# Optimization experiments

Hardware: AMD Instinct MI355X
Metric: run time of the kernel (lower is better)

## Reference

```python
import jax, jax.numpy as jnp
import numpy as np

B, T, D = 64, 512, 384
MAX_LEN = 4096


def setup_inputs() -> dict:
    key = jax.random.key(0)
    kx, kd = jax.random.split(key)
    x = jax.random.normal(kx, (B, T, D), dtype=jnp.float32)
    duration = jax.random.randint(kd, (B, T), 0, 8, dtype=jnp.int32)
    return {"x": x, "duration": duration, "max_len": MAX_LEN}


def reference(x, duration, max_len):
    # x: [B, T, D], duration: [B, T] int, max_len: python int
    # Cumsum trick replaces the per-row repeat_interleave + cat + pad:
    # token t of row b occupies output rows [csum[t-1], csum[t]).
    csum = jnp.cumsum(duration, axis=1)                       # [B, T]
    mel_len = csum[:, -1]                                     # [B]
    pos = jnp.arange(max_len, dtype=csum.dtype)               # [M]
    # For each output position m, index of source token: first t with csum[t] > m
    idx = jax.vmap(lambda c: jnp.searchsorted(c, pos, side="right"))(csum)  # [B, M]
    idx = jnp.minimum(idx, x.shape[1] - 1)
    out = jnp.take_along_axis(x, idx[:, :, None], axis=1)     # [B, M, D]
    mask = (pos[None, :] < mel_len[:, None])[:, :, None]      # [B, M, 1]
    out = jnp.where(mask, out, jnp.zeros((), dtype=out.dtype))
    return out, mel_len
```

## Files before the change

### kernel.cpp

```cpp
#include <hip/hip_runtime.h>


#define T_DIM 512
#define D_DIM 384
#define D4    (D_DIM / 4)
#define ROWS  32
#define BLOCK 512

__global__ __launch_bounds__(BLOCK) void length_regulator_kernel(
    const float* __restrict__ x,
    const int*   __restrict__ duration,
    float*       __restrict__ out,
    int B, int ML)
{
    __shared__ int s_csum[T_DIM];
    __shared__ int s_idx[ROWS];

    const int chunks_per_b = ML / ROWS;
    const int b     = blockIdx.x / chunks_per_b;
    const int chunk = blockIdx.x % chunks_per_b;
    const int row0  = chunk * ROWS;
    const int tid   = threadIdx.x;

    s_csum[tid] = duration[b * T_DIM + tid];
    __syncthreads();

    for (int off = 1; off < T_DIM; off <<= 1) {
        int v = (tid >= off) ? s_csum[tid - off] : 0;
        __syncthreads();
        s_csum[tid] += v;
        __syncthreads();
    }
    const int mel = s_csum[T_DIM - 1];

    if (tid < ROWS) {
        const int pos = row0 + tid;
        int idx;
        if (pos >= mel) {
            idx = -1;
        } else {
            int lo = 0, hi = T_DIM;
            while (lo < hi) {
                int mid = (lo + hi) >> 1;
                if (s_csum[mid] <= pos) lo = mid + 1; else hi = mid;
            }
            idx = (lo < T_DIM - 1) ? lo : (T_DIM - 1);
        }
        s_idx[tid] = idx;
    }
    __syncthreads();

    const float4* __restrict__ x4   = (const float4*)x;
    float4*       __restrict__ out4 = (float4*)out;
    const float4 zero = make_float4(0.f, 0.f, 0.f, 0.f);

    const long long out_base = ((long long)b * ML + row0) * D4;
    const long long x_base   = (long long)b * T_DIM * D4;

    #pragma unroll
    for (int i = 0; i < (ROWS * D4) / BLOCK; ++i) {
        const int flat = tid + i * BLOCK;
        const int r = flat / D4;
        const int j = flat - r * D4;
        const int t = s_idx[r];
        float4 v = (t < 0) ? zero : x4[x_base + (long long)t * D4 + j];
        out4[out_base + flat] = v;
    }

    if (chunk == 0 && tid == 0) {
        out[(long long)B * ML * D_DIM + b] = (float)mel;
    }
}

extern "C" void kernel_launch(void* const* d_in, const int* in_sizes, int n_in,
                              void* d_out, int out_size, void* d_ws, size_t ws_size,
                              hipStream_t stream) {
    const float* x   = (const float*)d_in[0];
    const int*   dur = (const int*)d_in[1];
    float*       out = (float*)d_out;

    const int B  = in_sizes[1] / T_DIM;
    const int ML = (out_size - B) / (B * D_DIM);

    const int grid = B * (ML / ROWS);
    hipLaunchKernelGGL(length_regulator_kernel, dim3(grid), dim3(BLOCK), 0, stream,
                       x, dur, out, B, ML);
}
```

Baseline: 472.2 us.

## Split into scan/index kernel and copy kernel with nontemporal stores

Before, every one of the 8192 blocks recomputed the full 512-element prefix sum for its batch row, which means redundant scans with many barriers per block. The scan and searchsorted now run once per batch in a separate kernel that writes gather indices to workspace. A lean copy kernel then reads those indices and gathers rows, writing output with nontemporal stores. This adds a second launch and a global round-trip for the index array, and it relies on the workspace being large enough to hold B*ML ints.

```diff
diff --git a/kernel.cpp b/kernel.cpp
--- a/kernel.cpp
+++ b/kernel.cpp
@@ -6,21 +6,19 @@
 #define D4    (D_DIM / 4)
 #define ROWS  32
 #define BLOCK 512
+#define ITER  ((ROWS * D4) / BLOCK)
 
-__global__ __launch_bounds__(BLOCK) void length_regulator_kernel(
-    const float* __restrict__ x,
-    const int*   __restrict__ duration,
-    float*       __restrict__ out,
-    int B, int ML)
+typedef float vfloat4 __attribute__((ext_vector_type(4)));
+
+__global__ __launch_bounds__(BLOCK) void lr_scan_idx_kernel(
+    const int* __restrict__ duration,
+    int*       __restrict__ idx,
+    float*     __restrict__ mel_out,
+    int ML)
 {
     __shared__ int s_csum[T_DIM];
-    __shared__ int s_idx[ROWS];
-
-    const int chunks_per_b = ML / ROWS;
-    const int b     = blockIdx.x / chunks_per_b;
-    const int chunk = blockIdx.x % chunks_per_b;
-    const int row0  = chunk * ROWS;
-    const int tid   = threadIdx.x;
+    const int b   = blockIdx.x;
+    const int tid = threadIdx.x;
 
     s_csum[tid] = duration[b * T_DIM + tid];
     __syncthreads();
@@ -32,43 +30,52 @@
         __syncthreads();
     }
     const int mel = s_csum[T_DIM - 1];
+    if (tid == 0) mel_out[b] = (float)mel;
 
-    if (tid < ROWS) {
-        const int pos = row0 + tid;
-        int idx;
-        if (pos >= mel) {
-            idx = -1;
+    for (int p = tid; p < ML; p += BLOCK) {
+        int v;
+        if (p >= mel) {
+            v = -1;
         } else {
             int lo = 0, hi = T_DIM;
             while (lo < hi) {
                 int mid = (lo + hi) >> 1;
-                if (s_csum[mid] <= pos) lo = mid + 1; else hi = mid;
+                if (s_csum[mid] <= p) lo = mid + 1; else hi = mid;
             }
-            idx = (lo < T_DIM - 1) ? lo : (T_DIM - 1);
+            v = (lo < T_DIM - 1) ? lo : (T_DIM - 1);
         }
-        s_idx[tid] = idx;
+        idx[b * ML + p] = v;
     }
-    __syncthreads();
+}
 
-    const float4* __restrict__ x4   = (const float4*)x;
-    float4*       __restrict__ out4 = (float4*)out;
-    const float4 zero = make_float4(0.f, 0.f, 0.f, 0.f);
+__global__ __launch_bounds__(BLOCK) void lr_copy_kernel(
+    const float* __restrict__ x,
+    const int*   __restrict__ idx,
+    float*       __restrict__ out,
+    int ML)
+{
+    const int chunks_per_b = ML / ROWS;
+    const int b     = blockIdx.x / chunks_per_b;
+    const int chunk = blockIdx.x % chunks_per_b;
+    const int row0  = chunk * ROWS;
+    const int tid   = threadIdx.x;
+
+    const vfloat4* __restrict__ x4   = (const vfloat4*)x;
+    vfloat4*       __restrict__ out4 = (vfloat4*)out;
 
     const long long out_base = ((long long)b * ML + row0) * D4;
     const long long x_base   = (long long)b * T_DIM * D4;
+    const int* __restrict__ idx_b = idx + b * ML + row0;
 
     #pragma unroll
-    for (int i = 0; i < (ROWS * D4) / BLOCK; ++i) {
+    for (int i = 0; i < ITER; ++i) {
         const int flat = tid + i * BLOCK;
         const int r = flat / D4;
         const int j = flat - r * D4;
-        const int t = s_idx[r];
-        float4 v = (t < 0) ? zero : x4[x_base + (long long)t * D4 + j];
-        out4[out_base + flat] = v;
-    }
-
-    if (chunk == 0 && tid == 0) {
-        out[(long long)B * ML * D_DIM + b] = (float)mel;
+        const int t = idx_b[r];
+        vfloat4 v = (vfloat4)(0.f, 0.f, 0.f, 0.f);
+        if (t >= 0) v = x4[x_base + (long long)t * D4 + j];
+        __builtin_nontemporal_store(v, &out4[out_base + flat]);
     }
 }
 
@@ -78,11 +85,17 @@
     const float* x   = (const float*)d_in[0];
     const int*   dur = (const int*)d_in[1];
     float*       out = (float*)d_out;
+    int*         idx = (int*)d_ws;
 
     const int B  = in_sizes[1] / T_DIM;
     const int ML = (out_size - B) / (B * D_DIM);
 
+    float* mel_out = out + (long long)B * ML * D_DIM;
+
+    hipLaunchKernelGGL(lr_scan_idx_kernel, dim3(B), dim3(BLOCK), 0, stream,
+                       dur, idx, mel_out, ML);
+
     const int grid = B * (ML / ROWS);
-    hipLaunchKernelGGL(length_regulator_kernel, dim3(grid), dim3(BLOCK), 0, stream,
-                       x, dur, out, B, ML);
+    hipLaunchKernelGGL(lr_copy_kernel, dim3(grid), dim3(BLOCK), 0, stream,
+                       x, idx, out, ML);
 }
```

Result: faster. 439.7 us (-6.9%).
